# Optimization experiments

Measured on AMD Instinct MI355X. Metric: run time of the kernel, lower is better.

Reference implementation:

```python
import jax, jax.numpy as jnp
import numpy as np
from jax import lax

HW = 256

def setup_inputs() -> dict:
    key = jax.random.key(0)
    k1, k2, k3 = jax.random.split(key, 3)
    B, C = 8, 64
    x1 = jax.random.normal(k1, (B, C, HW, HW), dtype=jnp.float32)
    x2 = jax.random.normal(k2, (B, C, HW, HW), dtype=jnp.float32)
    w = jnp.ones((1, 1, 3, 3), dtype=jnp.float32) / 9.0  # fixed box filter
    b = jax.random.normal(k3, (1,), dtype=jnp.float32) * 0.1  # conv bias
    return {"x1": x1, "x2": x2, "w": w, "b": b}

def _box_conv(y, w, b):
    # y: [B,1,H,W] ; 3x3 conv, stride 1, pad 1, plus bias
    out = lax.conv_general_dilated(
        y, w, window_strides=(1, 1), padding=[(1, 1), (1, 1)],
        dimension_numbers=("NCHW", "OIHW", "NCHW"))
    return out + b.reshape(1, -1, 1, 1)

def reference(x1, x2, w, b):
    # channel-wise L1 norm -> [B,1,H,W]
    n1 = jnp.sum(jnp.abs(x1), axis=-3).reshape(-1, 1, HW, HW)
    n2 = jnp.sum(jnp.abs(x2), axis=-3).reshape(-1, 1, HW, HW)
    c1 = _box_conv(n1, w, b)
    c2 = _box_conv(n2, w, b)
    denom = c1 + c2
    return x1 * c1 / denom + x2 * c2 / denom
```

## Files before the change

kernel.cpp:

```cpp
#include <hip/hip_runtime.h>

#define HWD 256
#define HW2 (HWD * HWD)
#define NB 8
#define NC 64
#define PLANE4 (HW2 / 4)

typedef float floatx4 __attribute__((ext_vector_type(4)));

__global__ void norms_kernel(const float* __restrict__ x1,
                             const float* __restrict__ x2,
                             float* __restrict__ n1,
                             float* __restrict__ n2) {
    const int s = threadIdx.x & 63;
    const int g = threadIdx.x >> 6;
    const int blk = blockIdx.x;
    const int b = blk >> 8;
    const int p = ((blk & 255) << 6) + s;

    const size_t base = (size_t)b * NC * PLANE4 + (size_t)g * 16 * PLANE4 + p;
    const float4* x1v = (const float4*)x1 + base;
    const float4* x2v = (const float4*)x2 + base;

    float4 a1 = make_float4(0.f, 0.f, 0.f, 0.f);
    float4 a2 = make_float4(0.f, 0.f, 0.f, 0.f);

#pragma unroll
    for (int c = 0; c < 16; ++c) {
        float4 v1 = x1v[(size_t)c * PLANE4];
        float4 v2 = x2v[(size_t)c * PLANE4];
        a1.x += fabsf(v1.x); a1.y += fabsf(v1.y);
        a1.z += fabsf(v1.z); a1.w += fabsf(v1.w);
        a2.x += fabsf(v2.x); a2.y += fabsf(v2.y);
        a2.z += fabsf(v2.z); a2.w += fabsf(v2.w);
    }

    __shared__ float4 l1[4][64];
    __shared__ float4 l2[4][64];
    l1[g][s] = a1;
    l2[g][s] = a2;
    __syncthreads();

    const size_t oidx = (size_t)b * PLANE4 + p;
    if (g == 0) {
        float4 r0 = l1[0][s], r1 = l1[1][s], r2 = l1[2][s], r3 = l1[3][s];
        float4 o;
        o.x = (r0.x + r1.x) + (r2.x + r3.x);
        o.y = (r0.y + r1.y) + (r2.y + r3.y);
        o.z = (r0.z + r1.z) + (r2.z + r3.z);
        o.w = (r0.w + r1.w) + (r2.w + r3.w);
        ((float4*)n1)[oidx] = o;
    } else if (g == 1) {
        float4 r0 = l2[0][s], r1 = l2[1][s], r2 = l2[2][s], r3 = l2[3][s];
        float4 o;
        o.x = (r0.x + r1.x) + (r2.x + r3.x);
        o.y = (r0.y + r1.y) + (r2.y + r3.y);
        o.z = (r0.z + r1.z) + (r2.z + r3.z);
        o.w = (r0.w + r1.w) + (r2.w + r3.w);
        ((float4*)n2)[oidx] = o;
    }
}

__global__ void conv_ratio_kernel(const float* __restrict__ n1,
                                  const float* __restrict__ n2,
                                  const float* __restrict__ w,
                                  const float* __restrict__ bias,
                                  float* __restrict__ r) {
    int t = blockIdx.x * blockDim.x + threadIdx.x;
    int b = t >> 16;
    int sp = t & (HW2 - 1);
    int y = sp >> 8;
    int x = sp & (HWD - 1);

    const float* p1 = n1 + (size_t)b * HW2;
    const float* p2 = n2 + (size_t)b * HW2;

    float s1 = 0.f, s2 = 0.f;
#pragma unroll
    for (int dy = -1; dy <= 1; ++dy) {
        int yy = y + dy;
        if (yy < 0 || yy >= HWD) continue;
#pragma unroll
        for (int dx = -1; dx <= 1; ++dx) {
            int xx = x + dx;
            if (xx < 0 || xx >= HWD) continue;
            float wv = w[(dy + 1) * 3 + (dx + 1)];
            int o = yy * HWD + xx;
            s1 += wv * p1[o];
            s2 += wv * p2[o];
        }
    }
    float bv = bias[0];
    float c1 = s1 + bv;
    float c2 = s2 + bv;
    r[t] = c1 / (c1 + c2);
}

__global__ void blend_kernel(const float* __restrict__ x1,
                             const float* __restrict__ x2,
                             const float* __restrict__ r,
                             float* __restrict__ out) {
    int t = blockIdx.x * blockDim.x + threadIdx.x;
    int p = t & (PLANE4 - 1);
    int cg = (t >> 14) & 7;
    int b = t >> 17;

    float4 rv = ((const float4*)r)[(size_t)b * PLANE4 + p];
    float4 one_m;
    one_m.x = 1.f - rv.x; one_m.y = 1.f - rv.y;
    one_m.z = 1.f - rv.z; one_m.w = 1.f - rv.w;

    size_t base = ((size_t)b * NC + (size_t)cg * 8) * PLANE4 + p;
    const float4* x1v = (const float4*)x1 + base;
    const float4* x2v = (const float4*)x2 + base;
    floatx4* ov = (floatx4*)out + base;

#pragma unroll
    for (int c = 0; c < 8; ++c) {
        float4 v1 = x1v[(size_t)c * PLANE4];
        float4 v2 = x2v[(size_t)c * PLANE4];
        floatx4 o;
        o.x = v1.x * rv.x + v2.x * one_m.x;
        o.y = v1.y * rv.y + v2.y * one_m.y;
        o.z = v1.z * rv.z + v2.z * one_m.z;
        o.w = v1.w * rv.w + v2.w * one_m.w;
        __builtin_nontemporal_store(o, ov + (size_t)c * PLANE4);
    }
}

extern "C" void kernel_launch(void* const* d_in, const int* in_sizes, int n_in,
                              void* d_out, int out_size, void* d_ws, size_t ws_size,
                              hipStream_t stream) {
    const float* x1 = (const float*)d_in[0];
    const float* x2 = (const float*)d_in[1];
    const float* w  = (const float*)d_in[2];
    const float* bv = (const float*)d_in[3];
    float* out = (float*)d_out;

    float* n1 = (float*)d_ws;
    float* n2 = n1 + (size_t)NB * HW2;
    float* r  = n2 + (size_t)NB * HW2;

    const int block = 256;

    norms_kernel<<<NB * (PLANE4 / 64), block, 0, stream>>>(x1, x2, n1, n2);
    conv_ratio_kernel<<<NB * HW2 / block, block, 0, stream>>>(n1, n2, w, bv, r);
    blend_kernel<<<NB * (NC / 8) * PLANE4 / block, block, 0, stream>>>(x1, x2, r, out);
}
```

Measured before the change: 359.0 us.

## Batch norm loads, vectorize conv over 4 pixels, grid-stride blend kernel

The norms kernel now issues four channel loads for each input before accumulating, so more memory requests are in flight. The conv/ratio kernel has each thread compute four adjacent outputs from float4 row loads plus halo scalars, and writes a float4 ratio. The blend kernel changes from 8 channels per thread to a flat, fully coalesced index with 4 elements per thread across a fixed grid, so r is re-read per element instead of being reused across channels. The aim is to raise memory-level parallelism in these bandwidth-bound passes, at the cost of more r loads in blend.

After: 361.4 us. No clear change (+0.7%).

```diff
diff --git a/kernel.cpp b/kernel.cpp
--- a/kernel.cpp
+++ b/kernel.cpp
@@ -26,13 +26,19 @@
     float4 a2 = make_float4(0.f, 0.f, 0.f, 0.f);
 
 #pragma unroll
-    for (int c = 0; c < 16; ++c) {
-        float4 v1 = x1v[(size_t)c * PLANE4];
-        float4 v2 = x2v[(size_t)c * PLANE4];
-        a1.x += fabsf(v1.x); a1.y += fabsf(v1.y);
-        a1.z += fabsf(v1.z); a1.w += fabsf(v1.w);
-        a2.x += fabsf(v2.x); a2.y += fabsf(v2.y);
-        a2.z += fabsf(v2.z); a2.w += fabsf(v2.w);
+    for (int c0 = 0; c0 < 16; c0 += 4) {
+        float4 v1[4], v2[4];
+#pragma unroll
+        for (int j = 0; j < 4; ++j) v1[j] = x1v[(size_t)(c0 + j) * PLANE4];
+#pragma unroll
+        for (int j = 0; j < 4; ++j) v2[j] = x2v[(size_t)(c0 + j) * PLANE4];
+#pragma unroll
+        for (int j = 0; j < 4; ++j) {
+            a1.x += fabsf(v1[j].x); a1.y += fabsf(v1[j].y);
+            a1.z += fabsf(v1[j].z); a1.w += fabsf(v1[j].w);
+            a2.x += fabsf(v2[j].x); a2.y += fabsf(v2[j].y);
+            a2.z += fabsf(v2[j].z); a2.w += fabsf(v2[j].w);
+        }
     }
 
     __shared__ float4 l1[4][64];
@@ -67,64 +73,87 @@
                                   const float* __restrict__ bias,
                                   float* __restrict__ r) {
     int t = blockIdx.x * blockDim.x + threadIdx.x;
-    int b = t >> 16;
-    int sp = t & (HW2 - 1);
-    int y = sp >> 8;
-    int x = sp & (HWD - 1);
+    int b = t >> 14;
+    int sp = t & ((HW2 / 4) - 1);
+    int y = sp >> 6;
+    int x0 = (sp & 63) << 2;
 
     const float* p1 = n1 + (size_t)b * HW2;
     const float* p2 = n2 + (size_t)b * HW2;
 
-    float s1 = 0.f, s2 = 0.f;
+    float o1[4] = {0.f, 0.f, 0.f, 0.f};
+    float o2[4] = {0.f, 0.f, 0.f, 0.f};
+
 #pragma unroll
     for (int dy = -1; dy <= 1; ++dy) {
         int yy = y + dy;
         if (yy < 0 || yy >= HWD) continue;
+        const float* r1 = p1 + yy * HWD;
+        const float* r2 = p2 + yy * HWD;
+        float4 m1 = *(const float4*)(r1 + x0);
+        float4 m2 = *(const float4*)(r2 + x0);
+        float e1[6], e2[6];
+        e1[0] = (x0 > 0) ? r1[x0 - 1] : 0.f;
+        e2[0] = (x0 > 0) ? r2[x0 - 1] : 0.f;
+        e1[1] = m1.x; e1[2] = m1.y; e1[3] = m1.z; e1[4] = m1.w;
+        e2[1] = m2.x; e2[2] = m2.y; e2[3] = m2.z; e2[4] = m2.w;
+        e1[5] = (x0 + 4 < HWD) ? r1[x0 + 4] : 0.f;
+        e2[5] = (x0 + 4 < HWD) ? r2[x0 + 4] : 0.f;
+        const float* wr = w + (dy + 1) * 3;
 #pragma unroll
-        for (int dx = -1; dx <= 1; ++dx) {
-            int xx = x + dx;
-            if (xx < 0 || xx >= HWD) continue;
-            float wv = w[(dy + 1) * 3 + (dx + 1)];
-            int o = yy * HWD + xx;
-            s1 += wv * p1[o];
-            s2 += wv * p2[o];
+        for (int j = 0; j < 4; ++j) {
+#pragma unroll
+            for (int k = 0; k < 3; ++k) {
+                o1[j] += wr[k] * e1[j + k];
+                o2[j] += wr[k] * e2[j + k];
+            }
         }
     }
+
     float bv = bias[0];
-    float c1 = s1 + bv;
-    float c2 = s2 + bv;
-    r[t] = c1 / (c1 + c2);
+    float4 out;
+    {
+        float c1 = o1[0] + bv, c2 = o2[0] + bv; out.x = c1 / (c1 + c2);
+    }
+    {
+        float c1 = o1[1] + bv, c2 = o2[1] + bv; out.y = c1 / (c1 + c2);
+    }
+    {
+        float c1 = o1[2] + bv, c2 = o2[2] + bv; out.z = c1 / (c1 + c2);
+    }
+    {
+        float c1 = o1[3] + bv, c2 = o2[3] + bv; out.w = c1 / (c1 + c2);
+    }
+    ((float4*)r)[t] = out;
 }
+
+#define BLEND_BLOCKS 8192
+#define BLEND_STRIDE ((size_t)BLEND_BLOCKS * 256)
 
 __global__ void blend_kernel(const float* __restrict__ x1,
                              const float* __restrict__ x2,
                              const float* __restrict__ r,
                              float* __restrict__ out) {
-    int t = blockIdx.x * blockDim.x + threadIdx.x;
-    int p = t & (PLANE4 - 1);
-    int cg = (t >> 14) & 7;
-    int b = t >> 17;
-
-    float4 rv = ((const float4*)r)[(size_t)b * PLANE4 + p];
-    float4 one_m;
-    one_m.x = 1.f - rv.x; one_m.y = 1.f - rv.y;
-    one_m.z = 1.f - rv.z; one_m.w = 1.f - rv.w;
-
-    size_t base = ((size_t)b * NC + (size_t)cg * 8) * PLANE4 + p;
-    const float4* x1v = (const float4*)x1 + base;
-    const float4* x2v = (const float4*)x2 + base;
-    floatx4* ov = (floatx4*)out + base;
+    size_t idx = (size_t)blockIdx.x * 256 + threadIdx.x;
+    const float4* x1v = (const float4*)x1;
+    const float4* x2v = (const float4*)x2;
+    const float4* rv4 = (const float4*)r;
+    floatx4* ov = (floatx4*)out;
 
 #pragma unroll
-    for (int c = 0; c < 8; ++c) {
-        float4 v1 = x1v[(size_t)c * PLANE4];
-        float4 v2 = x2v[(size_t)c * PLANE4];
+    for (int k = 0; k < 4; ++k) {
+        size_t i = idx + (size_t)k * BLEND_STRIDE;
+        int b = (int)(i >> 20);
+        int p = (int)(i & (PLANE4 - 1));
+        float4 rv = rv4[((size_t)b << 14) + p];
+        float4 v1 = x1v[i];
+        float4 v2 = x2v[i];
         floatx4 o;
-        o.x = v1.x * rv.x + v2.x * one_m.x;
-        o.y = v1.y * rv.y + v2.y * one_m.y;
-        o.z = v1.z * rv.z + v2.z * one_m.z;
-        o.w = v1.w * rv.w + v2.w * one_m.w;
-        __builtin_nontemporal_store(o, ov + (size_t)c * PLANE4);
+        o.x = v1.x * rv.x + v2.x * (1.f - rv.x);
+        o.y = v1.y * rv.y + v2.y * (1.f - rv.y);
+        o.z = v1.z * rv.z + v2.z * (1.f - rv.z);
+        o.w = v1.w * rv.w + v2.w * (1.f - rv.w);
+        __builtin_nontemporal_store(o, ov + i);
     }
 }
 
@@ -144,6 +173,6 @@
     const int block = 256;
 
     norms_kernel<<<NB * (PLANE4 / 64), block, 0, stream>>>(x1, x2, n1, n2);
-    conv_ratio_kernel<<<NB * HW2 / block, block, 0, stream>>>(n1, n2, w, bv, r);
-    blend_kernel<<<NB * (NC / 8) * PLANE4 / block, block, 0, stream>>>(x1, x2, r, out);
+    conv_ratio_kernel<<<NB * HW2 / 4 / block, block, 0, stream>>>(n1, n2, w, bv, r);
+    blend_kernel<<<BLEND_BLOCKS, block, 0, stream>>>(x1, x2, r, out);
 }
```
